# Kernel tuning notes

Hardware: AMD Instinct MI355X
Metric: run time of the kernel (lower is better)

## Reference

```python
import jax, jax.numpy as jnp
import numpy as np

WH, WW = 8, 8            # window size
N = WH * WW              # tokens per window = 64
DIM = 512
HEADS = 16
NW = 64                  # windows per image (mask batch)
B = 1024                 # total windows = 16 images * 64 windows
CPB_HIDDEN = 512


def _make_buffers():
    # relative coords table for CPB-MLP: [1, 2*WH-1, 2*WW-1, 2]
    rch = np.arange(-(WH - 1), WH, dtype=np.float32)
    rcw = np.arange(-(WW - 1), WW, dtype=np.float32)
    table = np.stack(np.meshgrid(rch, rcw, indexing='ij'), axis=-1)[None]
    table[..., 0] /= (WH - 1)
    table[..., 1] /= (WW - 1)
    table *= 8.0
    table = np.sign(table) * np.log2(np.abs(table) + 1.0) / 3.0
    # relative position index: [N, N]
    coords = np.stack(np.meshgrid(np.arange(WH), np.arange(WW), indexing='ij'), 0).reshape(2, -1)
    rel = coords[:, :, None] - coords[:, None, :]      # [2, N, N]
    rel = rel.transpose(1, 2, 0).astype(np.int64)
    rel[..., 0] += WH - 1
    rel[..., 1] += WW - 1
    rel[..., 0] *= 2 * WW - 1
    idx = rel.sum(-1)
    return jnp.asarray(table, jnp.float32), jnp.asarray(idx, jnp.int32)


def setup_inputs() -> dict:
    key = jax.random.key(0)
    ks = jax.random.split(key, 8)
    table, idx = _make_buffers()
    return {
        'x': jax.random.normal(ks[0], (B, N, DIM), jnp.float32),
        'mask': jax.random.normal(ks[1], (NW, N, N), jnp.float32),
        'qkv_w': jax.random.normal(ks[2], (3 * DIM, DIM), jnp.float32) * 0.02,
        'q_bias': jnp.zeros((DIM,), jnp.float32),
        'v_bias': jnp.zeros((DIM,), jnp.float32),
        'logit_scale': jnp.full((HEADS, 1, 1), np.log(10.0), jnp.float32),
        'cpb_w1': jax.random.normal(ks[3], (CPB_HIDDEN, 2), jnp.float32) * 0.02,
        'cpb_b1': jnp.zeros((CPB_HIDDEN,), jnp.float32),
        'cpb_w2': jax.random.normal(ks[4], (HEADS, CPB_HIDDEN), jnp.float32) * 0.02,
        'proj_w': jax.random.normal(ks[5], (DIM, DIM), jnp.float32) * 0.02,
        'proj_b': jnp.zeros((DIM,), jnp.float32),
        'rel_coords_table': table,
        'rel_pos_index': idx,
    }


def _l2norm(t):
    n = jnp.sqrt(jnp.sum(t * t, axis=-1, keepdims=True))
    return t / jnp.maximum(n, 1e-12)


def reference(x, mask, qkv_w, q_bias, v_bias, logit_scale, cpb_w1, cpb_b1,
              cpb_w2, proj_w, proj_b, rel_coords_table, rel_pos_index):
    Bq, Nq, C = x.shape
    qkv_b = jnp.concatenate([q_bias, jnp.zeros_like(v_bias), v_bias])
    qkv = x @ qkv_w.T + qkv_b                                  # [B, N, 3C]
    qkv = qkv.reshape(Bq, Nq, 3, HEADS, C // HEADS).transpose(2, 0, 3, 1, 4)
    q, k, v = qkv[0], qkv[1], qkv[2]                           # [B, H, N, D]
    attn = jnp.einsum('bhnd,bhmd->bhnm', _l2norm(q), _l2norm(k))
    scale = jnp.exp(jnp.minimum(logit_scale, jnp.log(jnp.float32(100.0))))
    attn = attn * scale                                        # [B, H, N, N]
    # CPB-MLP relative position bias
    hidden = jax.nn.relu(rel_coords_table @ cpb_w1.T + cpb_b1)  # [1, 2WH-1, 2WW-1, 512]
    bias_table = (hidden @ cpb_w2.T).reshape(-1, HEADS)         # [(2WH-1)(2WW-1), H]
    rel_bias = bias_table[rel_pos_index.reshape(-1)].reshape(Nq, Nq, HEADS)
    rel_bias = 16.0 * jax.nn.sigmoid(rel_bias.transpose(2, 0, 1))  # [H, N, N]
    attn = attn + rel_bias[None]
    nW = mask.shape[0]
    attn = attn.reshape(Bq // nW, nW, HEADS, Nq, Nq) + mask[None, :, None]
    attn = jax.nn.softmax(attn.reshape(Bq, HEADS, Nq, Nq), axis=-1)
    out = jnp.einsum('bhnm,bhmd->bhnd', attn, v)
    out = out.transpose(0, 2, 1, 3).reshape(Bq, Nq, C)
    return out @ proj_w.T + proj_b
```

## Files before the change

kernel.cpp:

```cpp
#include <hip/hip_runtime.h>
#include <hip/hip_bf16.h>

typedef __bf16 bf16;
typedef __bf16 bf16x8 __attribute__((ext_vector_type(8)));
typedef float floatx4 __attribute__((ext_vector_type(4)));

#define MFMA16(a, b, c) __builtin_amdgcn_mfma_f32_16x16x32_bf16((a), (b), (c), 0, 0, 0)

static constexpr long OFF_QKV   = 0;
static constexpr long OFF_XB    = 201326592;
static constexpr long OFF_WQKV  = 268435456;
static constexpr long OFF_WPROJ = 270008320;
static constexpr long OFF_BT    = 270532608;
static constexpr long OFF_RB    = 270548992;

__device__ __forceinline__ void load_lds16(const bf16* g, bf16* l) {
  __builtin_amdgcn_global_load_lds((const __attribute__((address_space(1))) void*)(g),
                                   (__attribute__((address_space(3))) void*)(l), 16, 0, 0);
}

__global__ __launch_bounds__(256) void cvt_f32_bf16(const float* __restrict__ src,
                                                    bf16* __restrict__ dst, int n8) {
  int i = blockIdx.x * 256 + threadIdx.x;
  if (i < n8) {
    const float4* s = (const float4*)src;
    float4 a = s[2 * i], b = s[2 * i + 1];
    bf16x8 o;
    o[0] = (bf16)a.x; o[1] = (bf16)a.y; o[2] = (bf16)a.z; o[3] = (bf16)a.w;
    o[4] = (bf16)b.x; o[5] = (bf16)b.y; o[6] = (bf16)b.z; o[7] = (bf16)b.w;
    ((bf16x8*)dst)[i] = o;
  }
}

__global__ __launch_bounds__(256) void cpb_mlp(const float* __restrict__ table,
                                               const float* __restrict__ w1,
                                               const float* __restrict__ b1,
                                               const float* __restrict__ w2,
                                               float* __restrict__ bias_table) {
  __shared__ float hid[512];
  const int e = blockIdx.x;
  const float t0 = table[e * 2 + 0], t1 = table[e * 2 + 1];
  for (int j = threadIdx.x; j < 512; j += 256) {
    float hv = t0 * w1[j * 2 + 0] + t1 * w1[j * 2 + 1] + b1[j];
    hid[j] = hv > 0.f ? hv : 0.f;
  }
  __syncthreads();
  const int hd = threadIdx.x >> 4, l = threadIdx.x & 15;
  float p = 0.f;
  for (int j = l; j < 512; j += 16) p += hid[j] * w2[hd * 512 + j];
  #pragma unroll
  for (int d = 8; d >= 1; d >>= 1) p += __shfl_xor(p, d, 16);
  if (l == 0) bias_table[e * 16 + hd] = p;
}

__global__ __launch_bounds__(256) void cpb_gather(const float* __restrict__ bias_table,
                                                  const int* __restrict__ idx,
                                                  float* __restrict__ rel_bias) {
  int f = blockIdx.x * 256 + threadIdx.x;
  int h = f >> 12, ij = f & 4095;
  float v = bias_table[idx[ij] * 16 + h];
  rel_bias[f] = 16.f / (1.f + __expf(-v));
}

template <int NN, bool QKV>
__global__ __launch_bounds__(256, 2) void gemm_bt(const bf16* __restrict__ A,
                                                  const bf16* __restrict__ Bt,
                                                  void* __restrict__ outv,
                                                  const float* __restrict__ bias_a,
                                                  const float* __restrict__ bias_b) {
  constexpr int K = 512;
  constexpr int nblk = NN / 128;
  __shared__ alignas(16) bf16 As[128 * 64];
  __shared__ alignas(16) bf16 Bs[128 * 64];
  const int tid = threadIdx.x;
  const int lane = tid & 63;
  const int wv = tid >> 6;
  const int bid = blockIdx.x;
  const int xcd = bid & 7;
  const int g = bid >> 3;
  const int mb = xcd * 64 + g / nblk;
  const int nb = g % nblk;
  const long m0 = (long)mb * 128;
  const int n0 = nb * 128;
  const int wm = (wv & 1) * 64;
  const int wn = (wv >> 1) * 64;
  const int cl = lane & 15;
  const int cq = lane >> 4;

  const floatx4 fzero = {0.f, 0.f, 0.f, 0.f};
  floatx4 acc[4][4];
  #pragma unroll
  for (int i = 0; i < 4; ++i)
    #pragma unroll
    for (int j = 0; j < 4; ++j) acc[i][j] = fzero;

  int srow[4], sc8[4];
  #pragma unroll
  for (int r = 0; r < 4; ++r) {
    int s = r * 256 + tid;
    srow[r] = s >> 3;
    sc8[r] = (s & 7) ^ (srow[r] & 7);
  }
  const int wbase = tid & ~63;

  for (int kt = 0; kt < K / 64; ++kt) {
    const int k0 = kt * 64;
    #pragma unroll
    for (int r = 0; r < 4; ++r) {
      const bf16* ga = A + (m0 + srow[r]) * K + (k0 + sc8[r] * 8);
      load_lds16(ga, &As[(r * 256 + wbase) * 8]);
      const bf16* gb = Bt + (long)(n0 + srow[r]) * K + (k0 + sc8[r] * 8);
      load_lds16(gb, &Bs[(r * 256 + wbase) * 8]);
    }
    __syncthreads();
    #pragma unroll
    for (int kk = 0; kk < 2; ++kk) {
      bf16x8 af[4], bfr[4];
      const int gg = kk * 4 + cq;
      #pragma unroll
      for (int t = 0; t < 4; ++t) {
        const int mr = wm + t * 16 + cl;
        af[t] = *(const bf16x8*)&As[(mr * 8 + (gg ^ (mr & 7))) * 8];
        const int nr = wn + t * 16 + cl;
        bfr[t] = *(const bf16x8*)&Bs[(nr * 8 + (gg ^ (nr & 7))) * 8];
      }
      #pragma unroll
      for (int i = 0; i < 4; ++i)
        #pragma unroll
        for (int j = 0; j < 4; ++j) acc[i][j] = MFMA16(af[i], bfr[j], acc[i][j]);
    }
    __syncthreads();
  }

  #pragma unroll
  for (int i = 0; i < 4; ++i) {
    #pragma unroll
    for (int j = 0; j < 4; ++j) {
      #pragma unroll
      for (int r = 0; r < 4; ++r) {
        const long grow = m0 + wm + i * 16 + cq * 4 + r;
        const int gcol = n0 + wn + j * 16 + cl;
        float v = acc[i][j][r];
        if constexpr (QKV) {
          float bias = (gcol < 512) ? bias_a[gcol]
                                    : ((gcol >= 1024) ? bias_b[gcol - 1024] : 0.f);
          ((bf16*)outv)[grow * NN + gcol] = (bf16)(v + bias);
        } else {
          ((float*)outv)[grow * NN + gcol] = v + bias_a[gcol];
        }
      }
    }
  }
}

__global__ __launch_bounds__(256, 5) void attn_kernel(const bf16* __restrict__ qkv,
                                                      const float* __restrict__ mask,
                                                      const float* __restrict__ lscale,
                                                      const float* __restrict__ rel_bias,
                                                      bf16* __restrict__ out) {
  const int bid = blockIdx.x;
  const int xcd = bid & 7;
  const int t = bid >> 3;
  const int p = xcd + ((t >> 1) << 3);
  const int b = p >> 3;
  const int h = ((p & 7) << 1) | (t & 1);
  const int wi = b & 63;
  const int tid = threadIdx.x;
  const int lane = tid & 63;
  const int wv = tid >> 6;
  const int cl = lane & 15;
  const int cq = lane >> 4;

  __shared__ alignas(16) bf16 smem[12544];
  bf16* qh_s = smem;
  bf16* ql_s = smem + 2560;
  bf16* kh_s = smem + 5120;
  bf16* kl_s = smem + 7680;
  bf16* vT   = smem + 10240;
  bf16* ps   = smem;

  {
    const int r = tid >> 2, seg = tid & 3;
    const bf16* base = qkv + (long)(b * 64 + r) * 1536 + h * 32 + seg * 8;
    float f[8], ss;
    bf16x8 hi, lo;

    bf16x8 qv = *(const bf16x8*)(base);
    ss = 0.f;
    #pragma unroll
    for (int j = 0; j < 8; ++j) { f[j] = (float)qv[j]; ss += f[j] * f[j]; }
    ss += __shfl_xor(ss, 1, 4); ss += __shfl_xor(ss, 2, 4);
    float s1 = 1.f / fmaxf(sqrtf(ss), 1e-12f);
    #pragma unroll
    for (int j = 0; j < 8; ++j) {
      float xn = f[j] * s1;
      bf16 xh = (bf16)xn;
      hi[j] = xh; lo[j] = (bf16)(xn - (float)xh);
    }
    *(bf16x8*)&qh_s[r * 40 + seg * 8] = hi;
    *(bf16x8*)&ql_s[r * 40 + seg * 8] = lo;

    bf16x8 kv = *(const bf16x8*)(base + 512);
    ss = 0.f;
    #pragma unroll
    for (int j = 0; j < 8; ++j) { f[j] = (float)kv[j]; ss += f[j] * f[j]; }
    ss += __shfl_xor(ss, 1, 4); ss += __shfl_xor(ss, 2, 4);
    s1 = 1.f / fmaxf(sqrtf(ss), 1e-12f);
    #pragma unroll
    for (int j = 0; j < 8; ++j) {
      float xn = f[j] * s1;
      bf16 xh = (bf16)xn;
      hi[j] = xh; lo[j] = (bf16)(xn - (float)xh);
    }
    *(bf16x8*)&kh_s[r * 40 + seg * 8] = hi;
    *(bf16x8*)&kl_s[r * 40 + seg * 8] = lo;

    bf16x8 vv = *(const bf16x8*)(base + 1024);
    #pragma unroll
    for (int j = 0; j < 8; ++j) vT[(seg * 8 + j) * 72 + r] = vv[j];
  }
  __syncthreads();

  const float sc = __expf(fminf(lscale[h], 4.6051701859880914f));

  const int mrow = wv * 16 + cl;
  const bf16x8 aqh = *(const bf16x8*)&qh_s[mrow * 40 + cq * 8];
  const bf16x8 aql = *(const bf16x8*)&ql_s[mrow * 40 + cq * 8];
  floatx4 sacc[4];
  #pragma unroll
  for (int nt = 0; nt < 4; ++nt) {
    const int nr = nt * 16 + cl;
    const bf16x8 bkh = *(const bf16x8*)&kh_s[nr * 40 + cq * 8];
    const bf16x8 bkl = *(const bf16x8*)&kl_s[nr * 40 + cq * 8];
    floatx4 a = {0.f, 0.f, 0.f, 0.f};
    a = MFMA16(aql, bkh, a);
    a = MFMA16(aqh, bkl, a);
    a = MFMA16(aqh, bkh, a);
    sacc[nt] = a;
  }
  __syncthreads();

  float pw[4][4];
  #pragma unroll
  for (int rg = 0; rg < 4; ++rg) {
    const int row = wv * 16 + cq * 4 + rg;
    const float* rbp = rel_bias + h * 4096 + row * 64;
    const float* mkp = mask + wi * 4096 + row * 64;
    float mxv = -1e30f;
    #pragma unroll
    for (int nt = 0; nt < 4; ++nt) {
      float s = sacc[nt][rg] * sc + rbp[nt * 16 + cl] + mkp[nt * 16 + cl];
      pw[rg][nt] = s;
      mxv = fmaxf(mxv, s);
    }
    #pragma unroll
    for (int d = 8; d >= 1; d >>= 1) mxv = fmaxf(mxv, __shfl_xor(mxv, d, 16));
    float sm = 0.f;
    #pragma unroll
    for (int nt = 0; nt < 4; ++nt) {
      float e = __expf(pw[rg][nt] - mxv);
      pw[rg][nt] = e;
      sm += e;
    }
    #pragma unroll
    for (int d = 8; d >= 1; d >>= 1) sm += __shfl_xor(sm, d, 16);
    const float inv = 1.f / sm;
    #pragma unroll
    for (int nt = 0; nt < 4; ++nt)
      ps[row * 72 + nt * 16 + cl] = (bf16)(pw[rg][nt] * inv);
  }

  floatx4 oacc[2];
  oacc[0] = (floatx4){0.f, 0.f, 0.f, 0.f};
  oacc[1] = (floatx4){0.f, 0.f, 0.f, 0.f};
  #pragma unroll
  for (int ks = 0; ks < 2; ++ks) {
    const bf16x8 ap = *(const bf16x8*)&ps[(wv * 16 + cl) * 72 + ks * 32 + cq * 8];
    #pragma unroll
    for (int nt = 0; nt < 2; ++nt) {
      const bf16x8 bv = *(const bf16x8*)&vT[(nt * 16 + cl) * 72 + ks * 32 + cq * 8];
      oacc[nt] = MFMA16(ap, bv, oacc[nt]);
    }
  }
  #pragma unroll
  for (int nt = 0; nt < 2; ++nt)
    #pragma unroll
    for (int rg = 0; rg < 4; ++rg) {
      const int row = wv * 16 + cq * 4 + rg;
      out[(long)(b * 64 + row) * 512 + h * 32 + nt * 16 + cl] = (bf16)oacc[nt][rg];
    }
}

extern "C" void kernel_launch(void* const* d_in, const int* in_sizes, int n_in,
                              void* d_out, int out_size, void* d_ws, size_t ws_size,
                              hipStream_t stream) {
  const float* x      = (const float*)d_in[0];
  const float* mask   = (const float*)d_in[1];
  const float* qkv_w  = (const float*)d_in[2];
  const float* q_bias = (const float*)d_in[3];
  const float* v_bias = (const float*)d_in[4];
  const float* lsc    = (const float*)d_in[5];
  const float* cpb_w1 = (const float*)d_in[6];
  const float* cpb_b1 = (const float*)d_in[7];
  const float* cpb_w2 = (const float*)d_in[8];
  const float* proj_w = (const float*)d_in[9];
  const float* proj_b = (const float*)d_in[10];
  const float* table  = (const float*)d_in[11];
  const int*   relidx = (const int*)d_in[12];

  char* ws = (char*)d_ws;
  bf16* qkvb   = (bf16*)(ws + OFF_QKV);
  bf16* xb     = (bf16*)(ws + OFF_XB);
  bf16* wqkv   = (bf16*)(ws + OFF_WQKV);
  bf16* wproj  = (bf16*)(ws + OFF_WPROJ);
  float* btab  = (float*)(ws + OFF_BT);
  float* rbias = (float*)(ws + OFF_RB);

  cvt_f32_bf16<<<16384, 256, 0, stream>>>(x, xb, 65536 * 512 / 8);
  cvt_f32_bf16<<<384, 256, 0, stream>>>(qkv_w, wqkv, 1536 * 512 / 8);
  cvt_f32_bf16<<<128, 256, 0, stream>>>(proj_w, wproj, 512 * 512 / 8);
  cpb_mlp<<<225, 256, 0, stream>>>(table, cpb_w1, cpb_b1, cpb_w2, btab);
  cpb_gather<<<256, 256, 0, stream>>>(btab, relidx, rbias);

  gemm_bt<1536, true><<<6144, 256, 0, stream>>>(xb, wqkv, (void*)qkvb, q_bias, v_bias);
  attn_kernel<<<16384, 256, 0, stream>>>(qkvb, mask, lsc, rbias, xb);
  gemm_bt<512, false><<<2048, 256, 0, stream>>>(xb, wproj, d_out, proj_b, nullptr);
}
```

Before: 571.5 us.

## Double-buffer GEMM LDS tiles and vectorize epilogue stores via swapped MFMA operands

The GEMM kernel now double-buffers its A/B LDS tiles, issuing the async global-to-LDS loads for the next K step before computing the current one, so memory latency overlaps with MFMA work and one barrier per iteration goes away. The MFMA operands are swapped in both the GEMM and the attention P·V product so each lane holds four consecutive output columns. The epilogues then write 4-wide vector stores with vectorized bias loads instead of scalar strided stores. Doubling LDS to 64KB per block may limit the two-blocks-per-CU occupancy target.

New measurement: 559.4 us. 2.1% less time.

```diff
diff --git a/kernel.cpp b/kernel.cpp
--- a/kernel.cpp
+++ b/kernel.cpp
@@ -2,6 +2,7 @@
 #include <hip/hip_bf16.h>
 
 typedef __bf16 bf16;
+typedef __bf16 bf16x4 __attribute__((ext_vector_type(4)));
 typedef __bf16 bf16x8 __attribute__((ext_vector_type(8)));
 typedef float floatx4 __attribute__((ext_vector_type(4)));
 
@@ -69,9 +70,10 @@
                                                   const float* __restrict__ bias_a,
                                                   const float* __restrict__ bias_b) {
   constexpr int K = 512;
+  constexpr int KT = K / 64;
   constexpr int nblk = NN / 128;
-  __shared__ alignas(16) bf16 As[128 * 64];
-  __shared__ alignas(16) bf16 Bs[128 * 64];
+  __shared__ alignas(16) bf16 As[2][128 * 64];
+  __shared__ alignas(16) bf16 Bs[2][128 * 64];
   const int tid = threadIdx.x;
   const int lane = tid & 63;
   const int wv = tid >> 6;
@@ -103,16 +105,23 @@
   }
   const int wbase = tid & ~63;
 
-  for (int kt = 0; kt < K / 64; ++kt) {
+  auto stage = [&](int buf, int kt) {
     const int k0 = kt * 64;
     #pragma unroll
     for (int r = 0; r < 4; ++r) {
       const bf16* ga = A + (m0 + srow[r]) * K + (k0 + sc8[r] * 8);
-      load_lds16(ga, &As[(r * 256 + wbase) * 8]);
+      load_lds16(ga, &As[buf][(r * 256 + wbase) * 8]);
       const bf16* gb = Bt + (long)(n0 + srow[r]) * K + (k0 + sc8[r] * 8);
-      load_lds16(gb, &Bs[(r * 256 + wbase) * 8]);
-    }
-    __syncthreads();
+      load_lds16(gb, &Bs[buf][(r * 256 + wbase) * 8]);
+    }
+  };
+
+  stage(0, 0);
+  __syncthreads();
+
+  int cur = 0;
+  for (int kt = 0; kt < KT; ++kt) {
+    if (kt + 1 < KT) stage(cur ^ 1, kt + 1);
     #pragma unroll
     for (int kk = 0; kk < 2; ++kk) {
       bf16x8 af[4], bfr[4];
@@ -120,34 +129,45 @@
       #pragma unroll
       for (int t = 0; t < 4; ++t) {
         const int mr = wm + t * 16 + cl;
-        af[t] = *(const bf16x8*)&As[(mr * 8 + (gg ^ (mr & 7))) * 8];
+        af[t] = *(const bf16x8*)&As[cur][(mr * 8 + (gg ^ (mr & 7))) * 8];
         const int nr = wn + t * 16 + cl;
-        bfr[t] = *(const bf16x8*)&Bs[(nr * 8 + (gg ^ (nr & 7))) * 8];
+        bfr[t] = *(const bf16x8*)&Bs[cur][(nr * 8 + (gg ^ (nr & 7))) * 8];
       }
       #pragma unroll
       for (int i = 0; i < 4; ++i)
         #pragma unroll
-        for (int j = 0; j < 4; ++j) acc[i][j] = MFMA16(af[i], bfr[j], acc[i][j]);
+        for (int j = 0; j < 4; ++j)
+          acc[i][j] = MFMA16(bfr[j], af[i], acc[i][j]);
     }
     __syncthreads();
-  }
-
+    cur ^= 1;
+  }
+
+  const int cq4 = cq * 4;
   #pragma unroll
   for (int i = 0; i < 4; ++i) {
+    const long m = m0 + wm + i * 16 + cl;
     #pragma unroll
     for (int j = 0; j < 4; ++j) {
-      #pragma unroll
-      for (int r = 0; r < 4; ++r) {
-        const long grow = m0 + wm + i * 16 + cq * 4 + r;
-        const int gcol = n0 + wn + j * 16 + cl;
-        float v = acc[i][j][r];
-        if constexpr (QKV) {
-          float bias = (gcol < 512) ? bias_a[gcol]
-                                    : ((gcol >= 1024) ? bias_b[gcol - 1024] : 0.f);
-          ((bf16*)outv)[grow * NN + gcol] = (bf16)(v + bias);
-        } else {
-          ((float*)outv)[grow * NN + gcol] = v + bias_a[gcol];
-        }
+      const int nbase = n0 + wn + j * 16 + cq4;
+      if constexpr (QKV) {
+        float4 bb = {0.f, 0.f, 0.f, 0.f};
+        if (nbase < 512) bb = *(const float4*)&bias_a[nbase];
+        else if (nbase >= 1024) bb = *(const float4*)&bias_b[nbase - 1024];
+        bf16x4 o;
+        o[0] = (bf16)(acc[i][j][0] + bb.x);
+        o[1] = (bf16)(acc[i][j][1] + bb.y);
+        o[2] = (bf16)(acc[i][j][2] + bb.z);
+        o[3] = (bf16)(acc[i][j][3] + bb.w);
+        *(bf16x4*)((bf16*)outv + m * NN + nbase) = o;
+      } else {
+        const float4 bb = *(const float4*)&bias_a[nbase];
+        float4 o;
+        o.x = acc[i][j][0] + bb.x;
+        o.y = acc[i][j][1] + bb.y;
+        o.z = acc[i][j][2] + bb.z;
+        o.w = acc[i][j][3] + bb.w;
+        *(float4*)((float*)outv + m * NN + nbase) = o;
       }
     }
   }
@@ -279,16 +299,17 @@
     #pragma unroll
     for (int nt = 0; nt < 2; ++nt) {
       const bf16x8 bv = *(const bf16x8*)&vT[(nt * 16 + cl) * 72 + ks * 32 + cq * 8];
-      oacc[nt] = MFMA16(ap, bv, oacc[nt]);
-    }
-  }
-  #pragma unroll
-  for (int nt = 0; nt < 2; ++nt)
-    #pragma unroll
-    for (int rg = 0; rg < 4; ++rg) {
-      const int row = wv * 16 + cq * 4 + rg;
-      out[(long)(b * 64 + row) * 512 + h * 32 + nt * 16 + cl] = (bf16)oacc[nt][rg];
-    }
+      oacc[nt] = MFMA16(bv, ap, oacc[nt]);
+    }
+  }
+  const long obase = (long)(b * 64 + wv * 16 + cl) * 512 + h * 32 + cq * 4;
+  #pragma unroll
+  for (int nt = 0; nt < 2; ++nt) {
+    bf16x4 o;
+    #pragma unroll
+    for (int r = 0; r < 4; ++r) o[r] = (bf16)oacc[nt][r];
+    *(bf16x4*)&out[obase + nt * 16] = o;
+  }
 }
 
 extern "C" void kernel_launch(void* const* d_in, const int* in_sizes, int n_in,
```
